# Optimization experiments

Measured on AMD Instinct MI355X. Metric: run time of the kernel, lower is better.

## Reference

```python
import jax, jax.numpy as jnp
import numpy as np

B, C, H, W = 512, 1, 280, 280
KS, S, P_PAD, F = 28, 28, 0, 16
HS = (H - KS + 2 * P_PAD) // S + 1  # 10
WS = (W - KS + 2 * P_PAD) // S + 1  # 10
P = HS * WS                          # 100 patches
OUT = 10


def setup_inputs() -> dict:
    key = jax.random.key(0)
    k1, k2, k3, k4, k5 = jax.random.split(key, 5)
    x = jax.random.normal(k1, (B, C, H, W), dtype=jnp.float32)
    weight = jax.random.normal(k2, (P * F, C, KS, KS), dtype=jnp.float32) * 0.05
    bias = jax.random.normal(k3, (P * F, C), dtype=jnp.float32) * 0.05
    dec_w = jax.random.normal(k4, (OUT, P * F * C), dtype=jnp.float32) * 0.05
    dec_b = jax.random.normal(k5, (OUT,), dtype=jnp.float32) * 0.05
    return {"x": x, "weight": weight, "bias": bias, "dec_w": dec_w, "dec_b": dec_b}


def _extract_patches(x):
    # x: (B, C, H+2p, W+2p) -> (B, P, C, KS, KS), patch order: row-major over (hs, ws)
    rows = jnp.arange(HS)[:, None] * S + jnp.arange(KS)[None, :]  # (HS, KS)
    cols = jnp.arange(WS)[:, None] * S + jnp.arange(KS)[None, :]  # (WS, KS)
    p = x[:, :, rows, :]            # (B, C, HS, KS, W)
    p = p[:, :, :, :, cols]         # (B, C, HS, KS, WS, KS)
    p = p.transpose(0, 2, 4, 1, 3, 5)  # (B, HS, WS, C, KS, KS)
    return p.reshape(B, P, C, KS, KS)


def reference(x, weight, bias, dec_w, dec_b):
    xp = jnp.pad(x, ((0, 0), (0, 0), (P_PAD, P_PAD), (P_PAD, P_PAD)))
    patches = _extract_patches(xp)                       # (B, P, C, KS, KS)
    # torch: x.repeat(1, f, ...) tiles patches f times; weight flat index i -> (f_idx, p_idx)
    w = weight.reshape(F, P, C, KS, KS)
    y = jnp.einsum('bpckl,fpckl->bfpc', patches, w)      # (B, F, P, C)
    y = y + bias.reshape(F, P, C)
    y = jax.nn.relu(y)
    y = y.reshape(B, F * P * C)
    return y @ dec_w.T + dec_b
```

## Files before the change

kernel.cpp:

```cpp
#include <hip/hip_runtime.h>
#include <stdint.h>

#define BATCH 512
#define HWIMG 78400
#define WROW  280
#define KSZ   28
#define PNUM  100
#define FNUM  16
#define ONUM  10

#define BT    64
#define CH    7
#define XF4   (BT * 28)
#define WF4   (FNUM * 28)

typedef __attribute__((address_space(1))) const void cg_void;
typedef __attribute__((address_space(3))) void lds_void;

__global__ __launch_bounds__(256) void init_out(const float* __restrict__ dec_b,
                                                float* __restrict__ out) {
    int i = blockIdx.x * 256 + threadIdx.x;
    if (i < BATCH * ONUM) out[i] = dec_b[i % ONUM];
}

__global__ __launch_bounds__(256) void lcn_fused(
    const float* __restrict__ x,
    const float* __restrict__ weight,
    const float* __restrict__ bias,
    const float* __restrict__ dec_w,
    float* __restrict__ out)
{
    __shared__ float4 lx[2][XF4];
    __shared__ float4 lw[2][WF4];

    const int t  = threadIdx.x;
    const int kg = t & 7;
    const int fg = (t >> 3) & 3;
    const int bg = t >> 5;
    const int bx = blockIdx.x;
    const int p  = bx >> 3;
    const int bt = bx & 7;
    const int pr = p / 10, pc = p % 10;
    const int b0 = bt * BT;

    const float* xs[7];
#pragma unroll
    for (int s = 0; s < 7; ++s) {
        int idx = s * 256 + t;
        int b  = idx / 28, rf = idx % 28;
        int r0 = rf / 7,   c4 = rf % 7;
        xs[s] = x + (size_t)(b0 + b) * HWIMG + (size_t)(pr * 28 + r0) * WROW
                  + pc * 28 + c4 * 4;
    }
    const int wi1 = 256 + (t < 192 ? t : t - 64);
    const float* ws0;
    const float* ws1;
    {
        int f = t / 28, rf = t % 28;
        ws0 = weight + ((size_t)(f * PNUM + p)) * 784 + rf * 4;
        f = wi1 / 28; rf = wi1 % 28;
        ws1 = weight + ((size_t)(f * PNUM + p)) * 784 + rf * 4;
    }

    auto issue_chunk = [&](int cc, int bb) {
#pragma unroll
        for (int s = 0; s < 7; ++s)
            __builtin_amdgcn_global_load_lds((cg_void*)(xs[s] + (size_t)cc * 4 * WROW),
                                             (lds_void*)&lx[bb][s * 256 + t], 16, 0, 0);
        __builtin_amdgcn_global_load_lds((cg_void*)(ws0 + (size_t)cc * 112),
                                         (lds_void*)&lw[bb][t], 16, 0, 0);
        __builtin_amdgcn_global_load_lds((cg_void*)(ws1 + (size_t)cc * 112),
                                         (lds_void*)&lw[bb][wi1], 16, 0, 0);
    };

    issue_chunk(0, 0);
    issue_chunk(1, 1);

    float acc[8][4];
#pragma unroll
    for (int i = 0; i < 8; ++i)
#pragma unroll
        for (int j = 0; j < 4; ++j) acc[i][j] = 0.f;

    const int kge = (kg < 7) ? kg : 0;

#pragma unroll
    for (int c = 0; c < CH; ++c) {
        const int buf = c & 1;
        if (c < CH - 1) asm volatile("s_waitcnt vmcnt(9)" ::: "memory");
        else            asm volatile("s_waitcnt vmcnt(0)" ::: "memory");
        __builtin_amdgcn_s_barrier();
        asm volatile("" ::: "memory");

#pragma unroll
        for (int m = 0; m < 4; ++m) {
            float4 wv[4];
#pragma unroll
            for (int j = 0; j < 4; ++j)
                wv[j] = lw[buf][(fg * 4 + j) * 28 + m * 7 + kge];
#pragma unroll
            for (int i = 0; i < 8; ++i) {
                float4 av = lx[buf][(bg * 8 + i) * 28 + m * 7 + kge];
#pragma unroll
                for (int j = 0; j < 4; ++j) {
                    acc[i][j] = fmaf(av.x, wv[j].x, acc[i][j]);
                    acc[i][j] = fmaf(av.y, wv[j].y, acc[i][j]);
                    acc[i][j] = fmaf(av.z, wv[j].z, acc[i][j]);
                    acc[i][j] = fmaf(av.w, wv[j].w, acc[i][j]);
                }
            }
        }

        asm volatile("" ::: "memory");
        __builtin_amdgcn_s_barrier();
        if (c + 2 < CH) issue_chunk(c + 2, buf);
    }

    const float km = (kg < 7) ? 1.f : 0.f;
#pragma unroll
    for (int i = 0; i < 8; ++i)
#pragma unroll
        for (int j = 0; j < 4; ++j) acc[i][j] *= km;

#pragma unroll
    for (int d = 1; d < 8; d <<= 1)
#pragma unroll
        for (int i = 0; i < 8; ++i)
#pragma unroll
            for (int j = 0; j < 4; ++j)
                acc[i][j] += __shfl_xor(acc[i][j], d, 64);

    float y[8][4];
#pragma unroll
    for (int j = 0; j < 4; ++j) {
        const float bs = bias[(fg * 4 + j) * PNUM + p];
#pragma unroll
        for (int i = 0; i < 8; ++i) {
            float v = acc[i][j] + bs;
            y[i][j] = v > 0.f ? v : 0.f;
        }
    }

    float po[8][2];
    const int  o0  = kg * 2;
    const bool act = (kg < 5);
    if (act) {
        float dwv[4][2];
#pragma unroll
        for (int j = 0; j < 4; ++j)
#pragma unroll
            for (int oo = 0; oo < 2; ++oo)
                dwv[j][oo] = dec_w[(size_t)(o0 + oo) * (PNUM * FNUM) + (fg * 4 + j) * PNUM + p];
#pragma unroll
        for (int i = 0; i < 8; ++i)
#pragma unroll
            for (int oo = 0; oo < 2; ++oo) {
                float s = 0.f;
#pragma unroll
                for (int j = 0; j < 4; ++j) s = fmaf(y[i][j], dwv[j][oo], s);
                po[i][oo] = s;
            }
    } else {
#pragma unroll
        for (int i = 0; i < 8; ++i) { po[i][0] = 0.f; po[i][1] = 0.f; }
    }

#pragma unroll
    for (int d = 8; d < 32; d <<= 1)
#pragma unroll
        for (int i = 0; i < 8; ++i)
#pragma unroll
            for (int oo = 0; oo < 2; ++oo)
                po[i][oo] += __shfl_xor(po[i][oo], d, 64);

    if (act && fg == 0) {
#pragma unroll
        for (int i = 0; i < 8; ++i)
#pragma unroll
            for (int oo = 0; oo < 2; ++oo)
                atomicAdd(&out[(size_t)(b0 + bg * 8 + i) * ONUM + o0 + oo], po[i][oo]);
    }
}

extern "C" void kernel_launch(void* const* d_in, const int* in_sizes, int n_in,
                              void* d_out, int out_size, void* d_ws, size_t ws_size,
                              hipStream_t stream) {
    const float* x     = (const float*)d_in[0];
    const float* w     = (const float*)d_in[1];
    const float* bias  = (const float*)d_in[2];
    const float* dec_w = (const float*)d_in[3];
    const float* dec_b = (const float*)d_in[4];
    float* out = (float*)d_out;

    init_out<<<(BATCH * ONUM + 255) / 256, 256, 0, stream>>>(dec_b, out);
    lcn_fused<<<(BATCH / BT) * PNUM, 256, 0, stream>>>(x, w, bias, dec_w, out);
}
```

Measured before the change: 256.5 us.

## Replace LDS double-buffered staging with direct global loads in small 64-thread blocks

```diff
diff --git a/kernel.cpp b/kernel.cpp
--- a/kernel.cpp
+++ b/kernel.cpp
@@ -4,18 +4,9 @@
 #define BATCH 512
 #define HWIMG 78400
 #define WROW  280
-#define KSZ   28
 #define PNUM  100
 #define FNUM  16
 #define ONUM  10
-
-#define BT    64
-#define CH    7
-#define XF4   (BT * 28)
-#define WF4   (FNUM * 28)
-
-typedef __attribute__((address_space(1))) const void cg_void;
-typedef __attribute__((address_space(3))) void lds_void;
 
 __global__ __launch_bounds__(256) void init_out(const float* __restrict__ dec_b,
                                                 float* __restrict__ out) {
@@ -23,58 +14,33 @@
     if (i < BATCH * ONUM) out[i] = dec_b[i % ONUM];
 }
 
-__global__ __launch_bounds__(256) void lcn_fused(
+__global__ __launch_bounds__(64, 4) void lcn_direct(
     const float* __restrict__ x,
     const float* __restrict__ weight,
     const float* __restrict__ bias,
     const float* __restrict__ dec_w,
     float* __restrict__ out)
 {
-    __shared__ float4 lx[2][XF4];
-    __shared__ float4 lw[2][WF4];
-
     const int t  = threadIdx.x;
     const int kg = t & 7;
     const int fg = (t >> 3) & 3;
     const int bg = t >> 5;
     const int bx = blockIdx.x;
-    const int p  = bx >> 3;
-    const int bt = bx & 7;
+    const int p    = bx >> 5;
+    const int bgrp = bx & 31;
+    const int b0   = bgrp * 16;
     const int pr = p / 10, pc = p % 10;
-    const int b0 = bt * BT;
+    const int kge = (kg < 7) ? kg : 0;
 
-    const float* xs[7];
+    const float* xb[8];
 #pragma unroll
-    for (int s = 0; s < 7; ++s) {
-        int idx = s * 256 + t;
-        int b  = idx / 28, rf = idx % 28;
-        int r0 = rf / 7,   c4 = rf % 7;
-        xs[s] = x + (size_t)(b0 + b) * HWIMG + (size_t)(pr * 28 + r0) * WROW
-                  + pc * 28 + c4 * 4;
-    }
-    const int wi1 = 256 + (t < 192 ? t : t - 64);
-    const float* ws0;
-    const float* ws1;
-    {
-        int f = t / 28, rf = t % 28;
-        ws0 = weight + ((size_t)(f * PNUM + p)) * 784 + rf * 4;
-        f = wi1 / 28; rf = wi1 % 28;
-        ws1 = weight + ((size_t)(f * PNUM + p)) * 784 + rf * 4;
-    }
-
-    auto issue_chunk = [&](int cc, int bb) {
+    for (int i = 0; i < 8; ++i)
+        xb[i] = x + (size_t)(b0 + bg * 8 + i) * HWIMG
+                  + (size_t)(pr * 28) * WROW + pc * 28 + kge * 4;
+    const float* wb[4];
 #pragma unroll
-        for (int s = 0; s < 7; ++s)
-            __builtin_amdgcn_global_load_lds((cg_void*)(xs[s] + (size_t)cc * 4 * WROW),
-                                             (lds_void*)&lx[bb][s * 256 + t], 16, 0, 0);
-        __builtin_amdgcn_global_load_lds((cg_void*)(ws0 + (size_t)cc * 112),
-                                         (lds_void*)&lw[bb][t], 16, 0, 0);
-        __builtin_amdgcn_global_load_lds((cg_void*)(ws1 + (size_t)cc * 112),
-                                         (lds_void*)&lw[bb][wi1], 16, 0, 0);
-    };
-
-    issue_chunk(0, 0);
-    issue_chunk(1, 1);
+    for (int j = 0; j < 4; ++j)
+        wb[j] = weight + (size_t)((fg * 4 + j) * PNUM + p) * 784 + kge * 4;
 
     float acc[8][4];
 #pragma unroll
@@ -82,25 +48,17 @@
 #pragma unroll
         for (int j = 0; j < 4; ++j) acc[i][j] = 0.f;
 
-    const int kge = (kg < 7) ? kg : 0;
-
-#pragma unroll
-    for (int c = 0; c < CH; ++c) {
-        const int buf = c & 1;
-        if (c < CH - 1) asm volatile("s_waitcnt vmcnt(9)" ::: "memory");
-        else            asm volatile("s_waitcnt vmcnt(0)" ::: "memory");
-        __builtin_amdgcn_s_barrier();
-        asm volatile("" ::: "memory");
-
+#pragma unroll 1
+    for (int c = 0; c < 7; ++c) {
 #pragma unroll
         for (int m = 0; m < 4; ++m) {
             float4 wv[4];
 #pragma unroll
             for (int j = 0; j < 4; ++j)
-                wv[j] = lw[buf][(fg * 4 + j) * 28 + m * 7 + kge];
+                wv[j] = *reinterpret_cast<const float4*>(wb[j] + m * 28);
 #pragma unroll
             for (int i = 0; i < 8; ++i) {
-                float4 av = lx[buf][(bg * 8 + i) * 28 + m * 7 + kge];
+                float4 av = *reinterpret_cast<const float4*>(xb[i] + m * WROW);
 #pragma unroll
                 for (int j = 0; j < 4; ++j) {
                     acc[i][j] = fmaf(av.x, wv[j].x, acc[i][j]);
@@ -110,10 +68,10 @@
                 }
             }
         }
-
-        asm volatile("" ::: "memory");
-        __builtin_amdgcn_s_barrier();
-        if (c + 2 < CH) issue_chunk(c + 2, buf);
+#pragma unroll
+        for (int i = 0; i < 8; ++i) xb[i] += 4 * WROW;
+#pragma unroll
+        for (int j = 0; j < 4; ++j) wb[j] += 4 * 28;
     }
 
     const float km = (kg < 7) ? 1.f : 0.f;
@@ -193,5 +151,5 @@
     float* out = (float*)d_out;
 
     init_out<<<(BATCH * ONUM + 255) / 256, 256, 0, stream>>>(dec_b, out);
-    lcn_fused<<<(BATCH / BT) * PNUM, 256, 0, stream>>>(x, w, bias, dec_w, out);
+    lcn_direct<<<(BATCH / 16) * PNUM, 64, 0, stream>>>(x, w, bias, dec_w, out);
 }
```

New measurement: 260.1 us. About the same (+1.4%).
